# Optimization experiments

Measured on AMD Instinct MI355X. Metric: run time of the kernel, lower is better.

Reference implementation:

```python
import jax, jax.numpy as jnp
import numpy as np

B, S, E, NH = 2, 1024, 2048, 16
DH = E // NH
EPS = 1e-6

def setup_inputs() -> dict:
    key = jax.random.key(0)
    ks = jax.random.split(key, 6)
    q = jax.random.normal(ks[0], (B, S, E), dtype=jnp.float32)
    k = jax.random.normal(ks[1], (B, S, E), dtype=jnp.float32)
    v = jax.random.normal(ks[2], (B, S, E), dtype=jnp.float32)
    Wi = jax.random.normal(ks[3], (3 * E, NH), dtype=jnp.float32) * 0.02
    bi = jax.random.normal(ks[4], (NH,), dtype=jnp.float32) * 0.1
    Wf = jax.random.normal(ks[5], (3 * E, NH), dtype=jnp.float32) * 0.02
    bf = jnp.linspace(3.0, 6.0, NH, dtype=jnp.float32)  # bias_linspace_initializer(3,6)
    ln_scale = jnp.ones((E,), dtype=jnp.float32)
    return {"q": q, "k": k, "v": v, "Wi": Wi, "bi": bi, "Wf": Wf, "bf": bf, "ln_scale": ln_scale}

def _mlstm_forward(q, k, v, Wi, bi, Wf, bf, ln_scale):
    b, s, e = q.shape
    nh = Wi.shape[1]
    dh = e // nh
    x = jnp.concatenate([q, k, v], axis=-1)                     # (B,S,3E)
    ig = (x @ Wi + bi).transpose(0, 2, 1)[..., None]            # (B,NH,S,1)
    fg = (x @ Wf + bf).transpose(0, 2, 1)[..., None]            # (B,NH,S,1)
    split = lambda t: t.reshape(b, s, nh, dh).transpose(0, 2, 1, 3)
    qh, kh, vh = split(q), split(k), split(v)                   # (B,NH,S,DH)
    # parallel_stabilized_simple backend
    log_f = jax.nn.log_sigmoid(fg)                              # (B,NH,S,1)
    log_f_cum = jnp.concatenate(
        [jnp.zeros((b, nh, 1, 1), q.dtype), jnp.cumsum(log_f, axis=2)], axis=2
    )                                                           # (B,NH,S+1,1)
    # D[i,j] = cumsum[i] - cumsum[j] on causal part
    fg_mat = log_f_cum - jnp.transpose(log_f_cum, (0, 1, 3, 2)) # (B,NH,S+1,S+1)
    ltr = jnp.tril(jnp.ones((s, s), dtype=bool))
    log_fg = jnp.where(ltr, fg_mat[:, :, 1:, 1:], -jnp.inf)     # (B,NH,S,S)
    log_D = log_fg + jnp.transpose(ig, (0, 1, 3, 2))            # + i_j per column
    max_log_D = jnp.max(log_D, axis=-1, keepdims=True)          # (B,NH,S,1)
    D = jnp.exp(log_D - max_log_D)
    qk = jnp.einsum('bhsd,bhtd->bhst', qh, kh) / jnp.sqrt(jnp.asarray(dh, q.dtype))
    C = qk * D                                                  # (B,NH,S,S)
    normalizer = jnp.maximum(jnp.abs(C.sum(-1, keepdims=True)), jnp.exp(-max_log_D))
    Cn = C / (normalizer + EPS)
    h = jnp.einsum('bhst,bhtd->bhsd', Cn, vh)                   # (B,NH,S,DH)
    # MultiHeadLayerNorm: normalize over DH per head, scale (no bias)
    mu = h.mean(-1, keepdims=True)
    var = ((h - mu) ** 2).mean(-1, keepdims=True)
    hn = (h - mu) * jax.lax.rsqrt(var + EPS)
    hn = hn * ln_scale.reshape(1, nh, 1, dh)
    return hn.transpose(0, 2, 1, 3).reshape(b, s, e)            # (B,S,E)

def reference(q, k, v, Wi, bi, Wf, bf, ln_scale):
    return _mlstm_forward(q, k, v, Wi, bi, Wf, bf, ln_scale)
```

## Files before the change

kernel.cpp:

```cpp
#include <hip/hip_runtime.h>
#include <hip/hip_bf16.h>

#define B_   2
#define S_   1024
#define E_   2048
#define NH_  16
#define DH_  128
#define EPS_ 1e-6f

using half8   = __attribute__((ext_vector_type(8))) _Float16;
using floatx4 = __attribute__((ext_vector_type(4))) float;

__device__ __forceinline__ half8 cvt8h(const float* __restrict__ p) {
    float4 a = *(const float4*)p;
    float4 b = *(const float4*)(p + 4);
    half8 r;
    r[0] = (_Float16)a.x; r[1] = (_Float16)a.y;
    r[2] = (_Float16)a.z; r[3] = (_Float16)a.w;
    r[4] = (_Float16)b.x; r[5] = (_Float16)b.y;
    r[6] = (_Float16)b.z; r[7] = (_Float16)b.w;
    return r;
}

__global__ __launch_bounds__(256, 4) void gates_kernel(
    const float* __restrict__ q, const float* __restrict__ k,
    const float* __restrict__ v, const float* __restrict__ Wi,
    const float* __restrict__ Wf, float* __restrict__ pre_i,
    float* __restrict__ pre_f, _Float16* __restrict__ qhg,
    _Float16* __restrict__ khg, _Float16* __restrict__ vtg)
{
    __shared__ __attribute__((aligned(16))) _Float16 xs[32 * 264];
    __shared__ __attribute__((aligned(16))) _Float16 wt[32 * 264];

    const int t    = threadIdx.x;
    const int w    = t >> 6, lane = t & 63, quad = lane >> 4, l15 = lane & 15;
    const int mw   = w & 1, nw = w >> 1;
    const int m0   = blockIdx.x * 32;
    const int by   = blockIdx.y;
    const int kbase = by * 768;
    const int bblk = m0 >> 10;
    const int s0   = m0 & 1023;

    floatx4 acc = {0.f, 0.f, 0.f, 0.f};

    for (int c = 0; c < 3; ++c) {
        __syncthreads();
        const int e0   = kbase + c * 256;
        const int tsel = e0 >> 11;
        const int el0  = e0 & 2047;
        const float* xb = (tsel == 0) ? q : (tsel == 1) ? k : v;
        _Float16* fout = (tsel == 0) ? qhg : khg;
        #pragma unroll
        for (int i = 0; i < 4; ++i) {
            int g = t + i * 256;
            int row = g >> 5, grp = g & 31;
            half8 s8 = cvt8h(xb + (size_t)(m0 + row) * E_ + el0 + grp * 8);
            *(half8*)(&xs[row * 264 + grp * 8]) = s8;
            if (tsel < 2) {
                int el = el0 + grp * 8;
                int h  = el >> 7, d = el & 127;
                *(half8*)(fout + ((size_t)(bblk * NH_ + h) * S_ + s0 + row) * DH_ + d) = s8;
            }
        }
        {
            const int kk = t;
            const float* wiRow = Wi + (size_t)(e0 + kk) * NH_;
            const float* wfRow = Wf + (size_t)(e0 + kk) * NH_;
            float wif[16], wff[16];
            #pragma unroll
            for (int i4 = 0; i4 < 4; ++i4) {
                float4 a = *(const float4*)(wiRow + i4 * 4);
                wif[i4*4+0]=a.x; wif[i4*4+1]=a.y; wif[i4*4+2]=a.z; wif[i4*4+3]=a.w;
                float4 b = *(const float4*)(wfRow + i4 * 4);
                wff[i4*4+0]=b.x; wff[i4*4+1]=b.y; wff[i4*4+2]=b.z; wff[i4*4+3]=b.w;
            }
            #pragma unroll
            for (int hh = 0; hh < 16; ++hh) wt[hh * 264 + kk]        = (_Float16)wif[hh];
            #pragma unroll
            for (int hh = 0; hh < 16; ++hh) wt[(16 + hh) * 264 + kk] = (_Float16)wff[hh];
        }
        __syncthreads();
        if (tsel == 2) {
            const int col = t;
            const int el  = el0 + col;
            const int h   = el >> 7, d = el & 127;
            _Float16 tmp[32];
            #pragma unroll
            for (int r = 0; r < 32; ++r) tmp[r] = xs[r * 264 + col];
            const size_t vo = ((size_t)(bblk * NH_ + h) * DH_ + d) * S_ + s0;
            #pragma unroll
            for (int i = 0; i < 4; ++i)
                *(half8*)(vtg + vo + i * 8) = *(half8*)(&tmp[i * 8]);
        }
        #pragma unroll
        for (int ks = 0; ks < 8; ++ks) {
            half8 af = *(const half8*)(&xs[(mw * 16 + l15) * 264 + ks * 32 + quad * 8]);
            half8 bw = *(const half8*)(&wt[(nw * 16 + l15) * 264 + ks * 32 + quad * 8]);
            acc = __builtin_amdgcn_mfma_f32_16x16x32_f16(af, bw, acc, 0, 0, 0);
        }
    }
    #pragma unroll
    for (int reg = 0; reg < 4; ++reg) {
        int m   = m0 + mw * 16 + quad * 4 + reg;
        int b   = m >> 10, s = m & 1023;
        int col = nw * 16 + l15;
        float vacc = acc[reg];
        if (col < 16)
            pre_i[((size_t)(by * 32 + b * NH_ + col)) * S_ + s] = vacc;
        else
            pre_f[((size_t)(by * 32 + b * NH_ + col - 16)) * S_ + s] = vacc;
    }
}

__global__ __launch_bounds__(1024, 1) void scan_kernel(
    const float* __restrict__ pre_i, const float* __restrict__ pre_f,
    float* __restrict__ Aj, float* __restrict__ Cq,
    float* __restrict__ NFo, const float* __restrict__ bi,
    const float* __restrict__ bfb)
{
    __shared__ float wsumF[16], wmaxA[16];
    const int bh   = blockIdx.x;
    const int h    = bh & 15;
    const int t    = threadIdx.x;
    const int lane = t & 63, wv = t >> 6;

    float igv = bi[h], x = bfb[h];
    #pragma unroll
    for (int y = 0; y < 8; ++y) {
        igv += pre_i[((size_t)(y * 32 + bh)) * S_ + t];
        x   += pre_f[((size_t)(y * 32 + bh)) * S_ + t];
    }
    float lfv = (x >= 0.f) ? -log1pf(__expf(-x)) : (x - log1pf(__expf(x)));

    float sc = lfv;
    #pragma unroll
    for (int off = 1; off < 64; off <<= 1) {
        float o = __shfl_up(sc, off);
        if (lane >= off) sc += o;
    }
    if (lane == 63) wsumF[wv] = sc;
    __syncthreads();
    float Foff = 0.f;
    for (int i = 0; i < wv; ++i) Foff += wsumF[i];
    float F = Foff + sc;
    float a = igv - F;

    float ms = a;
    #pragma unroll
    for (int off = 1; off < 64; off <<= 1) {
        float o = __shfl_up(ms, off);
        if (lane >= off) ms = fmaxf(ms, o);
    }
    if (lane == 63) wmaxA[wv] = ms;
    __syncthreads();
    float Moff = -3.0e38f;
    for (int i = 0; i < wv; ++i) Moff = fmaxf(Moff, wmaxA[i]);
    float M = fmaxf(Moff, ms);

    size_t o = (size_t)bh * S_ + t;
    Aj[o]  = a;
    Cq[o]  = -M;
    NFo[o] = expf(fminf(-(F + M), 80.f));
}

__global__ __launch_bounds__(256, 2) void attn_kernel(
    const _Float16* __restrict__ qh, const _Float16* __restrict__ kh,
    const _Float16* __restrict__ vtg, const float* __restrict__ Aj,
    const float* __restrict__ Cq, const float* __restrict__ NFi,
    const float* __restrict__ lnsc, float* __restrict__ out)
{
    __shared__ __attribute__((aligned(16))) _Float16 Ks[64 * 136];
    __shared__ __attribute__((aligned(16))) _Float16 Vt[128 * 72];
    __shared__ __attribute__((aligned(16))) _Float16 Pb[64 * 72];
    __shared__ float aj[64];
    __shared__ float lpart[2][2][32];
    __shared__ float spart[2][2][32];
    __shared__ float qpart[2][2][32];

    const int t    = threadIdx.x;
    const int w    = t >> 6, lane = t & 63, quad = lane >> 4, l15 = lane & 15;
    const int mw   = w & 1, nw = w >> 1;
    const int L    = blockIdx.x;
    int qi, bh;
    if (L < 256) { qi = L >> 5;                bh = L & 31; }
    else         { qi = 15 - ((L - 256) >> 5); bh = (L - 256) & 31; }
    const int b    = bh >> 4, h = bh & 15;
    const int q0   = qi * 64;
    const int krow = t >> 2, kd0 = (t & 3) * 32;
    const int vd   = t >> 1, vj0 = (t & 1) * 32;

    float ci_r[2][4], nfv_r[2][4];
    #pragma unroll
    for (int s = 0; s < 2; ++s)
        #pragma unroll
        for (int reg = 0; reg < 4; ++reg) {
            int rl = q0 + mw * 32 + s * 16 + quad * 4 + reg;
            ci_r[s][reg]  = Cq[(size_t)bh * S_ + rl];
            nfv_r[s][reg] = NFi[(size_t)bh * S_ + rl];
        }
    half8 aq[2][4];
    #pragma unroll
    for (int s = 0; s < 2; ++s) {
        const _Float16* qrow = qh + ((size_t)bh * S_ + q0 + mw * 32 + s * 16 + l15) * DH_;
        #pragma unroll
        for (int ks = 0; ks < 4; ++ks)
            aq[s][ks] = *(const half8*)(qrow + ks * 32 + quad * 8);
    }

    half8 kreg[4], vreg[4];
    float ajreg = 0.f;
    {
        const _Float16* kp = kh + ((size_t)bh * S_ + krow) * DH_ + kd0;
        const _Float16* vp = vtg + ((size_t)bh * DH_ + vd) * S_ + vj0;
        #pragma unroll
        for (int i = 0; i < 4; ++i) { kreg[i] = *(const half8*)(kp + i * 8);
                                      vreg[i] = *(const half8*)(vp + i * 8); }
    }
    if (t < 64) ajreg = Aj[(size_t)bh * S_ + t];

    #pragma unroll
    for (int i = 0; i < 4; ++i) {
        *(half8*)(&Ks[krow * 136 + kd0 + i * 8]) = kreg[i];
        *(half8*)(&Vt[vd * 72 + vj0 + i * 8])    = vreg[i];
    }
    if (t < 64) aj[t] = ajreg;
    __syncthreads();

    floatx4 acc_h[2][4];
    #pragma unroll
    for (int s = 0; s < 2; ++s)
        #pragma unroll
        for (int i = 0; i < 4; ++i) acc_h[s][i] = (floatx4){0.f, 0.f, 0.f, 0.f};
    float lrun[2][4] = {{0.f, 0.f, 0.f, 0.f}, {0.f, 0.f, 0.f, 0.f}};
    const float rscale = 0.08838834764831845f;

    for (int kt = 0; kt <= qi; ++kt) {
        if (kt < qi) {
            const int j0n = (kt + 1) * 64;
            const _Float16* kp = kh + ((size_t)bh * S_ + j0n + krow) * DH_ + kd0;
            const _Float16* vp = vtg + ((size_t)bh * DH_ + vd) * S_ + j0n + vj0;
            #pragma unroll
            for (int i = 0; i < 4; ++i) { kreg[i] = *(const half8*)(kp + i * 8);
                                          vreg[i] = *(const half8*)(vp + i * 8); }
            if (t < 64) ajreg = Aj[(size_t)bh * S_ + j0n + t];
        }

        const bool diag = (kt == qi);
        floatx4 sacc[2][2];
        #pragma unroll
        for (int s = 0; s < 2; ++s)
            #pragma unroll
            for (int n = 0; n < 2; ++n) sacc[s][n] = (floatx4){0.f, 0.f, 0.f, 0.f};
        if (!(diag && mw == 0 && nw == 1)) {
            __builtin_amdgcn_s_setprio(1);
            #pragma unroll
            for (int ks = 0; ks < 4; ++ks) {
                #pragma unroll
                for (int n = 0; n < 2; ++n) {
                    half8 bk = *(const half8*)(&Ks[(nw * 32 + n * 16 + l15) * 136 + ks * 32 + quad * 8]);
                    sacc[0][n] = __builtin_amdgcn_mfma_f32_16x16x32_f16(aq[0][ks], bk, sacc[0][n], 0, 0, 0);
                    sacc[1][n] = __builtin_amdgcn_mfma_f32_16x16x32_f16(aq[1][ks], bk, sacc[1][n], 0, 0, 0);
                }
            }
            __builtin_amdgcn_s_setprio(0);
        }
        #pragma unroll
        for (int n = 0; n < 2; ++n) {
            int jl = nw * 32 + n * 16 + l15;
            float a_j = aj[jl];
            #pragma unroll
            for (int s = 0; s < 2; ++s) {
                #pragma unroll
                for (int reg = 0; reg < 4; ++reg) {
                    int rloc = mw * 32 + s * 16 + quad * 4 + reg;
                    float p = 0.f;
                    if (!diag || (jl <= rloc))
                        p = sacc[s][n][reg] * rscale * __expf(fminf(ci_r[s][reg] + a_j, 0.f));
                    lrun[s][reg] += p;
                    Pb[rloc * 72 + jl] = (_Float16)p;
                }
            }
        }
        __syncthreads();

        if (kt < qi) {
            #pragma unroll
            for (int i = 0; i < 4; ++i)
                *(half8*)(&Ks[krow * 136 + kd0 + i * 8]) = kreg[i];
            if (t < 64) aj[t] = ajreg;
        }
        __builtin_amdgcn_s_setprio(1);
        #pragma unroll
        for (int ks2 = 0; ks2 < 2; ++ks2) {
            half8 ap0 = *(const half8*)(&Pb[(mw * 32 + l15) * 72 + ks2 * 32 + quad * 8]);
            half8 ap1 = *(const half8*)(&Pb[(mw * 32 + 16 + l15) * 72 + ks2 * 32 + quad * 8]);
            #pragma unroll
            for (int n = 0; n < 4; ++n) {
                half8 bv = *(const half8*)(&Vt[(nw * 64 + n * 16 + l15) * 72 + ks2 * 32 + quad * 8]);
                acc_h[0][n] = __builtin_amdgcn_mfma_f32_16x16x32_f16(ap0, bv, acc_h[0][n], 0, 0, 0);
                acc_h[1][n] = __builtin_amdgcn_mfma_f32_16x16x32_f16(ap1, bv, acc_h[1][n], 0, 0, 0);
            }
        }
        __builtin_amdgcn_s_setprio(0);
        __syncthreads();

        if (kt < qi) {
            #pragma unroll
            for (int i = 0; i < 4; ++i)
                *(half8*)(&Vt[vd * 72 + vj0 + i * 8]) = vreg[i];
        }
    }

    #pragma unroll
    for (int s = 0; s < 2; ++s)
        #pragma unroll
        for (int reg = 0; reg < 4; ++reg) {
            float l = lrun[s][reg];
            l += __shfl_xor(l, 1); l += __shfl_xor(l, 2);
            l += __shfl_xor(l, 4); l += __shfl_xor(l, 8);
            if (l15 == 0) lpart[nw][mw][s * 16 + quad * 4 + reg] = l;
        }
    __syncthreads();
    float inv_r[2][4];
    #pragma unroll
    for (int s = 0; s < 2; ++s)
        #pragma unroll
        for (int reg = 0; reg < 4; ++reg) {
            int rr = s * 16 + quad * 4 + reg;
            float ltot = lpart[0][mw][rr] + lpart[1][mw][rr];
            inv_r[s][reg] = 1.f / (fmaxf(fabsf(ltot), nfv_r[s][reg]) + EPS_);
        }
    #pragma unroll
    for (int s = 0; s < 2; ++s)
        #pragma unroll
        for (int reg = 0; reg < 4; ++reg) {
            float sum = 0.f, sq = 0.f;
            #pragma unroll
            for (int n = 0; n < 4; ++n) {
                float x = acc_h[s][n][reg] * inv_r[s][reg];
                sum += x; sq += x * x;
            }
            sum += __shfl_xor(sum, 1); sq += __shfl_xor(sq, 1);
            sum += __shfl_xor(sum, 2); sq += __shfl_xor(sq, 2);
            sum += __shfl_xor(sum, 4); sq += __shfl_xor(sq, 4);
            sum += __shfl_xor(sum, 8); sq += __shfl_xor(sq, 8);
            if (l15 == 0) {
                spart[nw][mw][s * 16 + quad * 4 + reg] = sum;
                qpart[nw][mw][s * 16 + quad * 4 + reg] = sq;
            }
        }
    __syncthreads();
    #pragma unroll
    for (int s = 0; s < 2; ++s)
        #pragma unroll
        for (int reg = 0; reg < 4; ++reg) {
            int rr   = s * 16 + quad * 4 + reg;
            float sum = spart[0][mw][rr] + spart[1][mw][rr];
            float sq  = qpart[0][mw][rr] + qpart[1][mw][rr];
            float mean = sum * (1.f / 128.f);
            float var  = fmaxf(sq * (1.f / 128.f) - mean * mean, 0.f);
            float rstd = rsqrtf(var + EPS_);
            int rl = q0 + mw * 32 + rr;
            size_t orow = ((size_t)b * S_ + rl) * E_ + h * DH_;
            #pragma unroll
            for (int n = 0; n < 4; ++n) {
                int d = nw * 64 + n * 16 + l15;
                out[orow + d] = (acc_h[s][n][reg] * inv_r[s][reg] - mean) * rstd * lnsc[h * DH_ + d];
            }
        }
}

extern "C" void kernel_launch(void* const* d_in, const int* in_sizes, int n_in,
                              void* d_out, int out_size, void* d_ws, size_t ws_size,
                              hipStream_t stream)
{
    const float* q    = (const float*)d_in[0];
    const float* k    = (const float*)d_in[1];
    const float* v    = (const float*)d_in[2];
    const float* Wi   = (const float*)d_in[3];
    const float* bi   = (const float*)d_in[4];
    const float* Wf   = (const float*)d_in[5];
    const float* bfb  = (const float*)d_in[6];
    const float* lnsc = (const float*)d_in[7];
    float* out        = (float*)d_out;

    const int NS  = B_ * NH_ * S_;
    float* pre_i = (float*)d_ws;
    float* pre_f = pre_i + 8 * NS;
    float* Aj    = pre_f + 8 * NS;
    float* Cq    = Aj + NS;
    float* NFa   = Cq + NS;
    _Float16* qh  = (_Float16*)(NFa + NS);
    _Float16* kh  = qh + (size_t)32 * S_ * DH_;
    _Float16* vtg = kh + (size_t)32 * S_ * DH_;

    gates_kernel<<<dim3(64, 8), 256, 0, stream>>>(q, k, v, Wi, Wf, pre_i, pre_f,
                                                  qh, kh, vtg);
    scan_kernel<<<dim3(32), 1024, 0, stream>>>(pre_i, pre_f, Aj, Cq, NFa, bi, bfb);
    attn_kernel<<<dim3(512), 256, 0, stream>>>(qh, kh, vtg, Aj, Cq, NFa, lnsc, out);
}
```

Before: 145.6 us.

## Fuse gate scan into attention kernel, recomputing per block

Drops the separate scan kernel. Each attention block now reduces the 8 split-K gate partials for its (b,h) over all 1024 positions, runs the log-sigmoid cumsum and running-max scans locally, and keeps the per-column a_j values in shared memory. This removes one kernel launch, the global round-trip for Aj/Cq/NF, and the per-tile Aj loads. In exchange, every one of the 16 query-tile blocks per head repeats the same scan work and adds two block syncs to its prologue.

```diff
diff --git a/kernel.cpp b/kernel.cpp
--- a/kernel.cpp
+++ b/kernel.cpp
@@ -112,67 +112,19 @@
     }
 }
 
-__global__ __launch_bounds__(1024, 1) void scan_kernel(
-    const float* __restrict__ pre_i, const float* __restrict__ pre_f,
-    float* __restrict__ Aj, float* __restrict__ Cq,
-    float* __restrict__ NFo, const float* __restrict__ bi,
-    const float* __restrict__ bfb)
-{
-    __shared__ float wsumF[16], wmaxA[16];
-    const int bh   = blockIdx.x;
-    const int h    = bh & 15;
-    const int t    = threadIdx.x;
-    const int lane = t & 63, wv = t >> 6;
-
-    float igv = bi[h], x = bfb[h];
-    #pragma unroll
-    for (int y = 0; y < 8; ++y) {
-        igv += pre_i[((size_t)(y * 32 + bh)) * S_ + t];
-        x   += pre_f[((size_t)(y * 32 + bh)) * S_ + t];
-    }
-    float lfv = (x >= 0.f) ? -log1pf(__expf(-x)) : (x - log1pf(__expf(x)));
-
-    float sc = lfv;
-    #pragma unroll
-    for (int off = 1; off < 64; off <<= 1) {
-        float o = __shfl_up(sc, off);
-        if (lane >= off) sc += o;
-    }
-    if (lane == 63) wsumF[wv] = sc;
-    __syncthreads();
-    float Foff = 0.f;
-    for (int i = 0; i < wv; ++i) Foff += wsumF[i];
-    float F = Foff + sc;
-    float a = igv - F;
-
-    float ms = a;
-    #pragma unroll
-    for (int off = 1; off < 64; off <<= 1) {
-        float o = __shfl_up(ms, off);
-        if (lane >= off) ms = fmaxf(ms, o);
-    }
-    if (lane == 63) wmaxA[wv] = ms;
-    __syncthreads();
-    float Moff = -3.0e38f;
-    for (int i = 0; i < wv; ++i) Moff = fmaxf(Moff, wmaxA[i]);
-    float M = fmaxf(Moff, ms);
-
-    size_t o = (size_t)bh * S_ + t;
-    Aj[o]  = a;
-    Cq[o]  = -M;
-    NFo[o] = expf(fminf(-(F + M), 80.f));
-}
-
 __global__ __launch_bounds__(256, 2) void attn_kernel(
     const _Float16* __restrict__ qh, const _Float16* __restrict__ kh,
-    const _Float16* __restrict__ vtg, const float* __restrict__ Aj,
-    const float* __restrict__ Cq, const float* __restrict__ NFi,
-    const float* __restrict__ lnsc, float* __restrict__ out)
+    const _Float16* __restrict__ vtg, const float* __restrict__ pre_i,
+    const float* __restrict__ pre_f, const float* __restrict__ bi,
+    const float* __restrict__ bfb, const float* __restrict__ lnsc,
+    float* __restrict__ out)
 {
     __shared__ __attribute__((aligned(16))) _Float16 Ks[64 * 136];
     __shared__ __attribute__((aligned(16))) _Float16 Vt[128 * 72];
     __shared__ __attribute__((aligned(16))) _Float16 Pb[64 * 72];
-    __shared__ float aj[64];
+    __shared__ __attribute__((aligned(16))) float ajAll[1024];
+    __shared__ float cq64[64], nf64[64];
+    __shared__ float wsum[4], wmax[4];
     __shared__ float lpart[2][2][32];
     __shared__ float spart[2][2][32];
     __shared__ float qpart[2][2][32];
@@ -189,14 +141,79 @@
     const int krow = t >> 2, kd0 = (t & 3) * 32;
     const int vd   = t >> 1, vj0 = (t & 1) * 32;
 
+    {
+        const int e4 = t * 4;
+        const float bih = bi[h], bfh = bfb[h];
+        float ig4[4] = {bih, bih, bih, bih};
+        float x4[4]  = {bfh, bfh, bfh, bfh};
+        #pragma unroll
+        for (int y = 0; y < 8; ++y) {
+            float4 pi = *(const float4*)(pre_i + ((size_t)(y * 32 + bh)) * S_ + e4);
+            float4 pf = *(const float4*)(pre_f + ((size_t)(y * 32 + bh)) * S_ + e4);
+            ig4[0] += pi.x; ig4[1] += pi.y; ig4[2] += pi.z; ig4[3] += pi.w;
+            x4[0]  += pf.x; x4[1]  += pf.y; x4[2]  += pf.z; x4[3]  += pf.w;
+        }
+        float lf[4], ls = 0.f;
+        #pragma unroll
+        for (int e = 0; e < 4; ++e) {
+            float x = x4[e];
+            float l = (x >= 0.f) ? -log1pf(__expf(-x)) : (x - log1pf(__expf(x)));
+            ls += l; lf[e] = ls;
+        }
+        float sc = ls;
+        #pragma unroll
+        for (int off = 1; off < 64; off <<= 1) {
+            float o = __shfl_up(sc, off);
+            if (lane >= off) sc += o;
+        }
+        float sexcl = sc - ls;
+        if (lane == 63) wsum[w] = sc;
+        __syncthreads();
+        float Foff = 0.f;
+        for (int i = 0; i < w; ++i) Foff += wsum[i];
+        float Fbase = Foff + sexcl;
+        float av[4], lm[4], am = -3.0e38f;
+        #pragma unroll
+        for (int e = 0; e < 4; ++e) {
+            float F = Fbase + lf[e];
+            float a = ig4[e] - F;
+            av[e] = a; am = fmaxf(am, a); lm[e] = am;
+        }
+        *(float4*)(&ajAll[e4]) = *(float4*)av;
+        float msc = am;
+        #pragma unroll
+        for (int off = 1; off < 64; off <<= 1) {
+            float o = __shfl_up(msc, off);
+            if (lane >= off) msc = fmaxf(msc, o);
+        }
+        float mprev = __shfl_up(msc, 1);
+        float mexcl = (lane == 0) ? -3.0e38f : mprev;
+        if (lane == 63) wmax[w] = msc;
+        __syncthreads();
+        float Moff = -3.0e38f;
+        for (int i = 0; i < w; ++i) Moff = fmaxf(Moff, wmax[i]);
+        float Mbase = fmaxf(Moff, mexcl);
+        #pragma unroll
+        for (int e = 0; e < 4; ++e) {
+            int s = e4 + e;
+            if (s >= q0 && s < q0 + 64) {
+                float M = fmaxf(Mbase, lm[e]);
+                float F = Fbase + lf[e];
+                cq64[s - q0] = -M;
+                nf64[s - q0] = expf(fminf(-(F + M), 80.f));
+            }
+        }
+    }
+    __syncthreads();
+
     float ci_r[2][4], nfv_r[2][4];
     #pragma unroll
     for (int s = 0; s < 2; ++s)
         #pragma unroll
         for (int reg = 0; reg < 4; ++reg) {
-            int rl = q0 + mw * 32 + s * 16 + quad * 4 + reg;
-            ci_r[s][reg]  = Cq[(size_t)bh * S_ + rl];
-            nfv_r[s][reg] = NFi[(size_t)bh * S_ + rl];
+            int rr = mw * 32 + s * 16 + quad * 4 + reg;
+            ci_r[s][reg]  = cq64[rr];
+            nfv_r[s][reg] = nf64[rr];
         }
     half8 aq[2][4];
     #pragma unroll
@@ -208,7 +225,6 @@
     }
 
     half8 kreg[4], vreg[4];
-    float ajreg = 0.f;
     {
         const _Float16* kp = kh + ((size_t)bh * S_ + krow) * DH_ + kd0;
         const _Float16* vp = vtg + ((size_t)bh * DH_ + vd) * S_ + vj0;
@@ -216,14 +232,11 @@
         for (int i = 0; i < 4; ++i) { kreg[i] = *(const half8*)(kp + i * 8);
                                       vreg[i] = *(const half8*)(vp + i * 8); }
     }
-    if (t < 64) ajreg = Aj[(size_t)bh * S_ + t];
-
     #pragma unroll
     for (int i = 0; i < 4; ++i) {
         *(half8*)(&Ks[krow * 136 + kd0 + i * 8]) = kreg[i];
         *(half8*)(&Vt[vd * 72 + vj0 + i * 8])    = vreg[i];
     }
-    if (t < 64) aj[t] = ajreg;
     __syncthreads();
 
     floatx4 acc_h[2][4];
@@ -242,7 +255,6 @@
             #pragma unroll
             for (int i = 0; i < 4; ++i) { kreg[i] = *(const half8*)(kp + i * 8);
                                           vreg[i] = *(const half8*)(vp + i * 8); }
-            if (t < 64) ajreg = Aj[(size_t)bh * S_ + j0n + t];
         }
 
         const bool diag = (kt == qi);
@@ -267,7 +279,7 @@
         #pragma unroll
         for (int n = 0; n < 2; ++n) {
             int jl = nw * 32 + n * 16 + l15;
-            float a_j = aj[jl];
+            float a_j = ajAll[kt * 64 + jl];
             #pragma unroll
             for (int s = 0; s < 2; ++s) {
                 #pragma unroll
@@ -287,7 +299,6 @@
             #pragma unroll
             for (int i = 0; i < 4; ++i)
                 *(half8*)(&Ks[krow * 136 + kd0 + i * 8]) = kreg[i];
-            if (t < 64) aj[t] = ajreg;
         }
         __builtin_amdgcn_s_setprio(1);
         #pragma unroll
@@ -387,15 +398,12 @@
     const int NS  = B_ * NH_ * S_;
     float* pre_i = (float*)d_ws;
     float* pre_f = pre_i + 8 * NS;
-    float* Aj    = pre_f + 8 * NS;
-    float* Cq    = Aj + NS;
-    float* NFa   = Cq + NS;
-    _Float16* qh  = (_Float16*)(NFa + NS);
+    _Float16* qh  = (_Float16*)(pre_f + 8 * NS);
     _Float16* kh  = qh + (size_t)32 * S_ * DH_;
     _Float16* vtg = kh + (size_t)32 * S_ * DH_;
 
     gates_kernel<<<dim3(64, 8), 256, 0, stream>>>(q, k, v, Wi, Wf, pre_i, pre_f,
                                                   qh, kh, vtg);
-    scan_kernel<<<dim3(32), 1024, 0, stream>>>(pre_i, pre_f, Aj, Cq, NFa, bi, bfb);
-    attn_kernel<<<dim3(512), 256, 0, stream>>>(qh, kh, vtg, Aj, Cq, NFa, lnsc, out);
+    attn_kernel<<<dim3(512), 256, 0, stream>>>(qh, kh, vtg, pre_i, pre_f,
+                                               bi, bfb, lnsc, out);
 }
```

Measured after the change: 146.5 us. Within noise of the previous version (+0.6%).
